# Kernel optimization log

Hardware: AMD Instinct MI355X
Metric: run time of the kernel (lower is better)

The kernel has to match this reference:

```python
import jax, jax.numpy as jnp
import numpy as np

U = 50  # lstm units

def lstm_seq(x, Wx, Wh, b):
    # x: [B,S,D] -> h: [B,S,U], Keras LSTMCell gate order i,f,g,o
    B = x.shape[0]
    xz = jnp.einsum('bsd,dk->bsk', x, Wx) + b  # [B,S,4U]
    def step(carry, zt):
        h, c = carry
        z = zt + h @ Wh
        i, f, g, o = jnp.split(z, 4, axis=-1)
        c = jax.nn.sigmoid(f) * c + jax.nn.sigmoid(i) * jnp.tanh(g)
        h = jax.nn.sigmoid(o) * jnp.tanh(c)
        return (h, c), h
    init = (jnp.zeros((B, U), x.dtype), jnp.zeros((B, U), x.dtype))
    _, hs = jax.lax.scan(step, init, jnp.swapaxes(xz, 0, 1))
    return jnp.swapaxes(hs, 0, 1)

def bilstm(x, fWx, fWh, fb, bWx, bWh, bb):
    # Keras RNN(go_backwards=True) does NOT re-reverse outputs; concat as-is.
    fw = lstm_seq(x, fWx, fWh, fb)
    bw = lstm_seq(x[:, ::-1, :], bWx, bWh, bb)
    return jnp.concatenate([fw, bw], axis=-1)

def local_inference(x1e, m1, x2e, m2):
    # Literal translation: inputs are batch-first [B,S,D]; the TF code transposes
    # to [S,B,D] and batch-matmuls over the leading (seq) axis, so attention is
    # over the batch index at each timestep. A[s,i,j] = x1e[i,s]. x2e[j,s]
    A = jnp.einsum('isd,jsd->sij', x1e, x2e)
    m1t = m1.T  # [S,B]
    m2t = m2.T
    w2 = jnp.exp(A - jnp.max(A, axis=2, keepdims=True)) * m2t[:, None, :]
    alpha = w2 / (jnp.sum(w2, axis=-1, keepdims=True) + 1e-8)
    x1_dual = jnp.einsum('sij,jsd->isd', alpha, x2e)  # [B,S,D]
    A1 = A - jnp.max(A, axis=1, keepdims=True)
    w1 = jnp.exp(jnp.swapaxes(A1, 1, 2)) * m1t[:, None, :]
    beta = w1 / (jnp.sum(w1, axis=-1, keepdims=True) + 1e-8)
    x2_dual = jnp.einsum('sji,isd->jsd', beta, x1e)  # [B,S,D]
    return x1_dual, x2_dual

def esim_forward(x1, x2, emb, b1f_Wx, b1f_Wh, b1f_b, b1b_Wx, b1b_Wh, b1b_b,
                 dense_W, dense_b, b2f_Wx, b2f_Wh, b2f_b, b2b_Wx, b2b_Wh, b2b_b,
                 dense1_W, dense1_b, out_W, out_b):
    m1 = (x1 != 0).astype(jnp.float32)
    m2 = (x2 != 0).astype(jnp.float32)
    e1 = emb[x1] * m1[..., None]
    e2 = emb[x2] * m2[..., None]
    enc1 = bilstm(e1, b1f_Wx, b1f_Wh, b1f_b, b1b_Wx, b1b_Wh, b1b_b) * m1[..., None]
    enc2 = bilstm(e2, b1f_Wx, b1f_Wh, b1f_b, b1b_Wx, b1b_Wh, b1b_b) * m2[..., None]
    d1, d2 = local_inference(enc1, m1, enc2, m2)
    match1 = jnp.concatenate([enc1, d1, enc1 * d1, enc1 - d1], axis=2)
    match2 = jnp.concatenate([enc2, d2, enc2 * d2, enc2 - d2], axis=2)
    map1 = jax.nn.relu(match1 @ dense_W + dense_b)
    map2 = jax.nn.relu(match2 @ dense_W + dense_b)
    cmp1 = bilstm(map1, b2f_Wx, b2f_Wh, b2f_b, b2b_Wx, b2b_Wh, b2b_b)
    cmp2 = bilstm(map2, b2f_Wx, b2f_Wh, b2f_b, b2b_Wx, b2b_Wh, b2b_b)
    c1m = cmp1 * m1[..., None]
    c2m = cmp2 * m2[..., None]
    p1_sum = jnp.sum(c1m, axis=1) / jnp.sum(m1, axis=1)[:, None]
    p1_max = jnp.max(c1m, axis=1)
    p2_sum = jnp.sum(c2m, axis=1) / jnp.sum(m2, axis=1)[:, None]
    p2_max = jnp.max(c2m, axis=1)
    logit = jnp.concatenate([p1_sum, p1_max, p2_sum, p2_max], axis=1)
    logit = jnp.tanh(logit @ dense1_W + dense1_b)
    logit = logit @ out_W + out_b
    return jax.nn.softmax(logit, axis=-1)

def setup_inputs() -> dict:
    key = jax.random.key(0)
    ks = jax.random.split(key, 24)
    B, S, V, E = 128, 512, 20000, 50
    def w(k, shape, s=0.05):
        return jax.random.normal(k, shape, dtype=jnp.float32) * s
    return {
        'x1': jax.random.randint(ks[0], (B, S), 0, V, dtype=jnp.int32),
        'x2': jax.random.randint(ks[1], (B, S), 0, V, dtype=jnp.int32),
        'emb': jax.random.uniform(ks[2], (V, E), jnp.float32, -0.05, 0.05),
        'b1f_Wx': w(ks[3], (E, 4 * U)), 'b1f_Wh': w(ks[4], (U, 4 * U)), 'b1f_b': w(ks[5], (4 * U,)),
        'b1b_Wx': w(ks[6], (E, 4 * U)), 'b1b_Wh': w(ks[7], (U, 4 * U)), 'b1b_b': w(ks[8], (4 * U,)),
        'dense_W': w(ks[9], (400, 100), 0.02), 'dense_b': jnp.zeros((100,), jnp.float32),
        'b2f_Wx': w(ks[10], (100, 4 * U)), 'b2f_Wh': w(ks[11], (U, 4 * U)), 'b2f_b': w(ks[12], (4 * U,)),
        'b2b_Wx': w(ks[13], (100, 4 * U)), 'b2b_Wh': w(ks[14], (U, 4 * U)), 'b2b_b': w(ks[15], (4 * U,)),
        'dense1_W': w(ks[16], (400, 100), 0.02), 'dense1_b': jnp.zeros((100,), jnp.float32),
        'out_W': w(ks[17], (100, 2), 0.02), 'out_b': jnp.zeros((2,), jnp.float32),
    }

def reference(x1, x2, emb, b1f_Wx, b1f_Wh, b1f_b, b1b_Wx, b1b_Wh, b1b_b,
              dense_W, dense_b, b2f_Wx, b2f_Wh, b2f_b, b2b_Wx, b2b_Wh, b2b_b,
              dense1_W, dense1_b, out_W, out_b):
    return esim_forward(x1, x2, emb, b1f_Wx, b1f_Wh, b1f_b, b1b_Wx, b1b_Wh, b1b_b,
                        dense_W, dense_b, b2f_Wx, b2f_Wh, b2f_b, b2b_Wx, b2b_Wh, b2b_b,
                        dense1_W, dense1_b, out_W, out_b)
```

## Files before the change

### kernel.cpp

```cpp
#include <hip/hip_runtime.h>

#define TOKN 65536
#define SQ 512
#define BB 128
#define DD 100
#define APAD 132

typedef unsigned short bf16t;
typedef __attribute__((ext_vector_type(8))) short bf16x8;
typedef __attribute__((ext_vector_type(4))) float floatx4;
typedef __attribute__((ext_vector_type(2))) _Float16 half2t;

__device__ __forceinline__ float bf2f(bf16t v) {
  unsigned u = ((unsigned)v) << 16;
  return __uint_as_float(u);
}
__device__ __forceinline__ bf16t f2bf(float x) {
  unsigned u = __float_as_uint(x);
  unsigned r = u + 0x7FFFu + ((u >> 16) & 1u);
  return (bf16t)(r >> 16);
}
__device__ __forceinline__ float2 ldpair(const float* p) { return *(const float2*)p; }
__device__ __forceinline__ float2 ldpair(const bf16t* p) {
  unsigned u = *(const unsigned*)p;
  float2 r;
  r.x = __uint_as_float(u << 16);
  r.y = __uint_as_float(u & 0xFFFF0000u);
  return r;
}
__device__ __forceinline__ half2t u2h2(unsigned u) {
  union { unsigned u; half2t h; } x; x.u = u; return x.h;
}

__device__ __forceinline__ float sigm(float x) { return 1.f / (1.f + __expf(-x)); }
__device__ __forceinline__ float tanhx(float x) { return 1.f - 2.f / (1.f + __expf(2.f * x)); }

#if __has_builtin(__builtin_amdgcn_fdot2)
#define DOT2(hu, wu, acc) acc = __builtin_amdgcn_fdot2(u2h2(hu), u2h2(wu), acc, false);
#else
#define DOT2(hu, wu, acc) { half2t hh = u2h2(hu), ww = u2h2(wu); \
  acc = fmaf((float)hh[0], (float)ww[0], acc); \
  acc = fmaf((float)hh[1], (float)ww[1], acc); }
#endif

__global__ __launch_bounds__(256) void embed_kernel(
    const int* __restrict__ x1, const int* __restrict__ x2,
    const float* __restrict__ emb,
    bf16t* __restrict__ e1, bf16t* __restrict__ e2,
    float* __restrict__ m1, float* __restrict__ m2) {
  const int which = blockIdx.y;
  const int* __restrict__ x = which ? x2 : x1;
  bf16t* __restrict__ e = which ? e2 : e1;
  float* __restrict__ m = which ? m2 : m1;
  int idx = blockIdx.x * 256 + threadIdx.x;
  int t = idx >> 6, d = idx & 63;
  int tok = x[t];
  float mk = (tok != 0) ? 1.f : 0.f;
  float v = (d < 50) ? emb[tok * 50 + d] * mk : 0.f;
  e[idx] = f2bf(v);
  if (d == 0) m[t] = mk;
}

__global__ __launch_bounds__(256) void padzero_kernel(
    unsigned* __restrict__ p1, unsigned* __restrict__ p2) {
  int idx = blockIdx.x * 256 + threadIdx.x;
  if (idx >= TOKN * 14) return;
  int t = idx / 14, d = idx - t * 14;
  p1[(size_t)t * 64 + 50 + d] = 0u;
  p2[(size_t)t * 64 + 50 + d] = 0u;
}

__global__ __launch_bounds__(256) void wprep_kernel(
    const float* __restrict__ w1f, const float* __restrict__ w1b,
    const float* __restrict__ w2f, const float* __restrict__ w2b,
    const float* __restrict__ dW,
    const float* __restrict__ h1f, const float* __restrict__ h1b,
    const float* __restrict__ h2f, const float* __restrict__ h2b,
    bf16t* __restrict__ w1T, bf16t* __restrict__ w2T, bf16t* __restrict__ wdT,
    unsigned* __restrict__ whP) {
  int idx = blockIdx.x * 256 + threadIdx.x;
  int sec = blockIdx.y;
  if (sec == 0) {
    if (idx >= 2 * 208 * 64) return;
    int d = idx / (208 * 64), r = idx % (208 * 64);
    int n = r >> 6, k = r & 63;
    const float* W = d ? w1b : w1f;
    float v = (n < 200 && k < 50) ? W[k * 200 + n] : 0.f;
    w1T[idx] = f2bf(v);
  } else if (sec == 1) {
    if (idx >= 2 * 208 * 128) return;
    int d = idx / (208 * 128), r = idx % (208 * 128);
    int n = r >> 7, k = r & 127;
    const float* W = d ? w2b : w2f;
    float v = (n < 200 && k < 100) ? W[k * 200 + n] : 0.f;
    w2T[idx] = f2bf(v);
  } else if (sec == 2) {
    if (idx >= 128 * 384) return;
    int n = idx / 384, kv = idx % 384;
    int reg = kv >> 7, kk = kv & 127;
    float v = 0.f;
    if (n < 100 && kk < 100) {
      if (reg == 0) v = dW[kk * 100 + n] + dW[(300 + kk) * 100 + n];
      else if (reg == 1) v = dW[(100 + kk) * 100 + n] - dW[(300 + kk) * 100 + n];
      else v = dW[(200 + kk) * 100 + n];
    }
    wdT[idx] = f2bf(v);
  } else {
    if (idx >= 4 * 25 * 200) return;
    int sd = idx / 5000, r = idx % 5000;
    int k2 = r / 200, colx = r % 200;
    const float* W = (sd == 0) ? h1f : (sd == 1) ? h1b : (sd == 2) ? h2f : h2b;
    float v0 = W[(2 * k2) * 200 + colx];
    float v1 = W[(2 * k2 + 1) * 200 + colx];
    union { _Float16 h[2]; unsigned u; } p;
    p.h[0] = (_Float16)v0;
    p.h[1] = (_Float16)v1;
    whP[idx] = p.u;
  }
}

template <int KP>
__global__ __launch_bounds__(256) void xz_mfma(
    const bf16t* __restrict__ A1, const bf16t* __restrict__ A2,
    const bf16t* __restrict__ WT,
    const float* __restrict__ bf_, const float* __restrict__ bb_,
    bf16t* __restrict__ out) {
  const int combo = blockIdx.y;
  const bf16t* __restrict__ A = (combo < 2) ? A1 : A2;
  const bf16t* __restrict__ W = WT + (size_t)(combo & 1) * 208 * KP;
  const float* __restrict__ bias = (combo & 1) ? bb_ : bf_;
  bf16t* __restrict__ O = out + (size_t)combo * TOKN * 200;
  const int tid = threadIdx.x;
  const int wave = tid >> 6, lane = tid & 63;
  const int m0 = blockIdx.x * 64 + wave * 16;
  const int l15 = lane & 15, quad = lane >> 4;
  floatx4 acc[13];
#pragma unroll
  for (int nt = 0; nt < 13; ++nt) acc[nt] = (floatx4){0.f, 0.f, 0.f, 0.f};
  const bf16t* __restrict__ arow = A + (size_t)(m0 + l15) * KP + quad * 8;
  const bf16t* __restrict__ wb = W + (size_t)l15 * KP + quad * 8;
#pragma unroll
  for (int ks = 0; ks < KP / 32; ++ks) {
    bf16x8 a = *(const bf16x8*)(arow + ks * 32);
#pragma unroll
    for (int nt = 0; nt < 13; ++nt) {
      bf16x8 b = *(const bf16x8*)(wb + (size_t)nt * 16 * KP + ks * 32);
      acc[nt] = __builtin_amdgcn_mfma_f32_16x16x32_bf16(a, b, acc[nt], 0, 0, 0);
    }
  }
  const int crow = m0 + quad * 4;
  const int bidx = crow >> 9;
  const int trow = crow & 511;
#pragma unroll
  for (int nt = 0; nt < 13; ++nt) {
    int n = nt * 16 + l15;
    if (n < 200) {
      float bn = bias[n];
      union { bf16t h[4]; uint2 u2; } pk;
#pragma unroll
      for (int r = 0; r < 4; ++r) pk.h[r] = f2bf(acc[nt][r] + bn);
      *(uint2*)&O[((size_t)bidx * 200 + n) * SQ + trow] = pk.u2;
    }
  }
}

__global__ __launch_bounds__(256) void dense_mfma(
    const bf16t* __restrict__ enc1, const bf16t* __restrict__ enc2,
    const bf16t* __restrict__ d1b, const bf16t* __restrict__ d2b,
    const bf16t* __restrict__ wdT, const float* __restrict__ bias,
    bf16t* __restrict__ map1, bf16t* __restrict__ map2) {
  const int inp = blockIdx.y;
  const bf16t* __restrict__ E = inp ? enc2 : enc1;
  const bf16t* __restrict__ Db = inp ? d2b : d1b;
  bf16t* __restrict__ O = inp ? map2 : map1;
  const int tid = threadIdx.x;
  const int wave = tid >> 6, lane = tid & 63;
  const int m0 = blockIdx.x * 64 + wave * 16;
  const int l15 = lane & 15, quad = lane >> 4;
  floatx4 acc[8];
#pragma unroll
  for (int nt = 0; nt < 8; ++nt) acc[nt] = (floatx4){0.f, 0.f, 0.f, 0.f};
  const bf16t* __restrict__ erow = E + (size_t)(m0 + l15) * 128 + quad * 8;
  const bf16t* __restrict__ drow = Db + (size_t)(m0 + l15) * 128 + quad * 8;
  const bf16t* __restrict__ wb = wdT + (size_t)l15 * 384 + quad * 8;
#pragma unroll
  for (int ks = 0; ks < 4; ++ks) {
    bf16x8 ae = *(const bf16x8*)(erow + ks * 32);
    bf16x8 ad = *(const bf16x8*)(drow + ks * 32);
    bf16x8 aed;
#pragma unroll
    for (int q = 0; q < 8; ++q) {
      float pe = bf2f((bf16t)ae[q]);
      float pd = bf2f((bf16t)ad[q]);
      aed[q] = (short)f2bf(pe * pd);
    }
#pragma unroll
    for (int nt = 0; nt < 8; ++nt) {
      const bf16t* wn = wb + (size_t)nt * 16 * 384 + ks * 32;
      bf16x8 b0 = *(const bf16x8*)(wn);
      acc[nt] = __builtin_amdgcn_mfma_f32_16x16x32_bf16(ae, b0, acc[nt], 0, 0, 0);
      bf16x8 b1 = *(const bf16x8*)(wn + 128);
      acc[nt] = __builtin_amdgcn_mfma_f32_16x16x32_bf16(ad, b1, acc[nt], 0, 0, 0);
      bf16x8 b2 = *(const bf16x8*)(wn + 256);
      acc[nt] = __builtin_amdgcn_mfma_f32_16x16x32_bf16(aed, b2, acc[nt], 0, 0, 0);
    }
  }
  const int crow = m0 + quad * 4;
#pragma unroll
  for (int nt = 0; nt < 8; ++nt) {
    int n = nt * 16 + l15;
    float bn = (n < 100) ? bias[n] : 0.f;
#pragma unroll
    for (int r = 0; r < 4; ++r) {
      float v = (n < 100) ? fmaxf(acc[nt][r] + bn, 0.f) : 0.f;
      O[(size_t)(crow + r) * 128 + n] = f2bf(v);
    }
  }
}

__global__ __launch_bounds__(64)
__attribute__((amdgpu_waves_per_eu(1, 2)))
void lstm_scan(
    const bf16t* __restrict__ xzT,
    const unsigned* __restrict__ whPL,
    bf16t* __restrict__ out1, bf16t* __restrict__ out2,
    const float* __restrict__ m1, const float* __restrict__ m2,
    int hasMask) {
  const int blk = blockIdx.x;
  const int scan = blk >> 7;
  const int b = blk & 127;
  const int inp = scan >> 1;
  const int dir = scan & 1;
  const int u = threadIdx.x;
  const bool act_l = (u < 50);
  const int uc = act_l ? u : 0;
  const bf16t* __restrict__ xbase = xzT + ((size_t)scan * 128 + b) * 200 * SQ;
  const bf16t* __restrict__ xi = xbase + (size_t)uc * SQ;
  const bf16t* __restrict__ xf = xbase + (size_t)(50 + uc) * SQ;
  const bf16t* __restrict__ xg = xbase + (size_t)(100 + uc) * SQ;
  const bf16t* __restrict__ xo = xbase + (size_t)(150 + uc) * SQ;
  bf16t* __restrict__ outp = (inp ? out2 : out1) + (size_t)b * SQ * 128 + dir * 50;
  const float* __restrict__ mk = (inp ? m2 : m1) + b * SQ;
  __shared__ __align__(16) unsigned hbuf[2][32];

  const unsigned* __restrict__ wsrc = whPL + dir * 5000;
  unsigned wgt[4][25];
#pragma unroll
  for (int gg = 0; gg < 4; ++gg)
#pragma unroll
    for (int k2 = 0; k2 < 25; ++k2)
      wgt[gg][k2] = wsrc[k2 * 200 + gg * 50 + uc];
#pragma unroll
  for (int gg = 0; gg < 4; ++gg)
#pragma unroll
    for (int k2 = 0; k2 < 25; ++k2)
      asm volatile("" : "+v"(wgt[gg][k2]));

  ((unsigned*)hbuf)[u] = 0;
  float c = 0.f;
  const float4* mk4 = (const float4*)mk;

  uint4 zc0, zc1, zc2, zc3, zn0, zn1, zn2, zn3;
  {
    int r0 = dir ? (SQ - 8) : 0;
    int r1 = dir ? (SQ - 16) : 8;
    zc0 = *(const uint4*)(xi + r0); zn0 = *(const uint4*)(xi + r1);
    zc1 = *(const uint4*)(xf + r0); zn1 = *(const uint4*)(xf + r1);
    zc2 = *(const uint4*)(xg + r0); zn2 = *(const uint4*)(xg + r1);
    zc3 = *(const uint4*)(xo + r0); zn3 = *(const uint4*)(xo + r1);
  }

  for (int g8 = 0; g8 < SQ / 8; ++g8) {
    float zst[4][8];
    {
      uint4 cur[4] = {zc0, zc1, zc2, zc3};
#pragma unroll
      for (int gg = 0; gg < 4; ++gg) {
        unsigned dw[4] = {cur[gg].x, cur[gg].y, cur[gg].z, cur[gg].w};
#pragma unroll
        for (int p = 0; p < 4; ++p) {
          float lo = __uint_as_float(dw[p] << 16);
          float hi = __uint_as_float(dw[p] & 0xFFFF0000u);
          if (dir) { zst[gg][7 - 2 * p] = lo; zst[gg][6 - 2 * p] = hi; }
          else     { zst[gg][2 * p] = lo;     zst[gg][2 * p + 1] = hi; }
        }
      }
    }
    uint4 zf0 = zn0, zf1 = zn1, zf2 = zn2, zf3 = zn3;
    {
      int gnext = (g8 + 2 < SQ / 8) ? (g8 + 2) : (SQ / 8 - 1);
      int rn = dir ? (SQ - 8 - 8 * gnext) : (8 * gnext);
      zn0 = *(const uint4*)(xi + rn);
      zn1 = *(const uint4*)(xf + rn);
      zn2 = *(const uint4*)(xg + rn);
      zn3 = *(const uint4*)(xo + rn);
    }
    float mva[8];
    if (hasMask) {
      float4 ma = mk4[2 * g8], mb = mk4[2 * g8 + 1];
      mva[0] = ma.x; mva[1] = ma.y; mva[2] = ma.z; mva[3] = ma.w;
      mva[4] = mb.x; mva[5] = mb.y; mva[6] = mb.z; mva[7] = mb.w;
    }
    bf16t hs8[8];
#pragma unroll
    for (int j = 0; j < 8; ++j) {
      const int par = j & 1;
      const uint4* hp = (const uint4*)&hbuf[par][0];
      uint4 q0 = hp[0], q1 = hp[1], q2 = hp[2], q3 = hp[3], q4 = hp[4], q5 = hp[5];
      unsigned qL = hbuf[par][24];
      unsigned hd[25] = {q0.x, q0.y, q0.z, q0.w, q1.x, q1.y, q1.z, q1.w,
                         q2.x, q2.y, q2.z, q2.w, q3.x, q3.y, q3.z, q3.w,
                         q4.x, q4.y, q4.z, q4.w, q5.x, q5.y, q5.z, q5.w, qL};
      float res[4];
#pragma unroll
      for (int gg = 0; gg < 4; ++gg) {
        float a0 = zst[gg][j], a1 = 0.f;
#pragma unroll
        for (int k2 = 0; k2 < 24; k2 += 2) {
          DOT2(hd[k2], wgt[gg][k2], a0)
          DOT2(hd[k2 + 1], wgt[gg][k2 + 1], a1)
        }
        DOT2(hd[24], wgt[gg][24], a0)
        res[gg] = a0 + a1;
      }
      float ai = sigm(res[0]);
      float af = sigm(res[1]);
      float ag = tanhx(res[2]);
      float ao = sigm(res[3]);
      c = af * c + ai * ag;
      float hn = ao * tanhx(c);
      if (act_l) {
        ((_Float16*)&hbuf[par ^ 1][0])[u] = (_Float16)hn;
        float mv = hasMask ? mva[j] : 1.f;
        hs8[j] = f2bf(hn * mv);
      }
    }
    if (act_l) {
      int t0 = 8 * g8;
#pragma unroll
      for (int j = 0; j < 8; ++j)
        outp[(size_t)(t0 + j) * 128 + u] = hs8[j];
    }
    zc0 = zf0; zc1 = zf1; zc2 = zf2; zc3 = zf3;
  }
}

__global__ __launch_bounds__(256) void attn_kernel(
    const bf16t* __restrict__ enc1, const bf16t* __restrict__ enc2,
    const float* __restrict__ m1, const float* __restrict__ m2,
    bf16t* __restrict__ d1b, bf16t* __restrict__ d2b) {
  const int s = blockIdx.x;
  const int tid = threadIdx.x;
  __shared__ __align__(16) float E1[BB][DD];
  __shared__ __align__(16) float E2[BB + 1][DD];
  __shared__ __align__(16) float Ah[64][APAD];
  __shared__ float mk1[BB], mk2[BB];
  __shared__ float rden[64];

  for (int idx = tid; idx < BB * 50; idx += 256) {
    int i = idx / 50, dp = idx - i * 50;
    float2 v1 = ldpair(enc1 + ((size_t)i * SQ + s) * 128 + 2 * dp);
    E1[i][2 * dp] = v1.x;
    E1[i][2 * dp + 1] = v1.y;
    float2 v2 = ldpair(enc2 + ((size_t)i * SQ + s) * 128 + 2 * dp);
    E2[i][2 * dp] = v2.x;
    E2[i][2 * dp + 1] = v2.y;
  }
  if (tid < BB) {
    mk1[tid] = m1[tid * SQ + s];
    mk2[tid] = m2[tid * SQ + s];
  }
  __syncthreads();

  const int ti = tid >> 4, tjj = tid & 15;
  const int xj = tid & 127;
  const int xd0 = (tid >> 7) * 50;
  float N[50];
#pragma unroll
  for (int q = 0; q < 50; ++q) N[q] = 0.f;
  float Dacc = 0.f, M = -1e30f;

  for (int half = 0; half < 2; ++half) {
    const int r0 = half * 64;
    float acc[4][8];
#pragma unroll
    for (int ii = 0; ii < 4; ++ii)
#pragma unroll
      for (int jj = 0; jj < 8; ++jj) acc[ii][jj] = 0.f;
    for (int k = 0; k < DD; k += 4) {
      float4 a4[4], b4[8];
#pragma unroll
      for (int ii = 0; ii < 4; ++ii)
        a4[ii] = *(const float4*)&E1[r0 + 4 * ti + ii][k];
#pragma unroll
      for (int jj = 0; jj < 8; ++jj)
        b4[jj] = *(const float4*)&E2[tjj + 16 * jj][k];
#pragma unroll
      for (int ii = 0; ii < 4; ++ii)
#pragma unroll
        for (int jj = 0; jj < 8; ++jj)
          acc[ii][jj] += a4[ii].x * b4[jj].x + a4[ii].y * b4[jj].y +
                         a4[ii].z * b4[jj].z + a4[ii].w * b4[jj].w;
    }
#pragma unroll
    for (int ii = 0; ii < 4; ++ii)
#pragma unroll
      for (int jj = 0; jj < 8; ++jj)
        Ah[4 * ti + ii][tjj + 16 * jj] = acc[ii][jj];
    __syncthreads();

    {
      float lm = M;
      for (int i = 0; i < 64; ++i) lm = fmaxf(lm, Ah[i][xj]);
      float scale = __expf(M - lm);
      Dacc *= scale;
#pragma unroll
      for (int q = 0; q < 50; ++q) N[q] *= scale;
      for (int i = 0; i < 64; ++i) {
        float p = __expf(Ah[i][xj] - lm) * mk1[r0 + i];
        Dacc += p;
        const float2* e1p = (const float2*)&E1[r0 + i][xd0];
#pragma unroll
        for (int q = 0; q < 25; ++q) {
          float2 ev = e1p[q];
          N[2 * q] += p * ev.x;
          N[2 * q + 1] += p * ev.y;
        }
      }
      M = lm;
    }
    __syncthreads();

    {
      int row = tid >> 2, seg = tid & 3;
      float mx = -1e30f;
      for (int q = 0; q < 32; ++q) mx = fmaxf(mx, Ah[row][seg + 4 * q]);
      mx = fmaxf(mx, __shfl_xor(mx, 1));
      mx = fmaxf(mx, __shfl_xor(mx, 2));
      float sm = 0.f;
      for (int q = 0; q < 32; ++q) {
        int jc = seg + 4 * q;
        float p = __expf(Ah[row][jc] - mx) * mk2[jc];
        Ah[row][jc] = p;
        sm += p;
      }
      sm += __shfl_xor(sm, 1);
      sm += __shfl_xor(sm, 2);
      if (seg == 0) rden[row] = sm + 1e-8f;
    }
    __syncthreads();

    {
      float o[4][8];
#pragma unroll
      for (int ii = 0; ii < 4; ++ii)
#pragma unroll
        for (int jj = 0; jj < 8; ++jj) o[ii][jj] = 0.f;
      for (int jb = 0; jb < BB; ++jb) {
        float pv[4], ev[8];
#pragma unroll
        for (int ii = 0; ii < 4; ++ii) pv[ii] = Ah[4 * ti + ii][jb];
#pragma unroll
        for (int jj = 0; jj < 8; ++jj) ev[jj] = E2[jb][tjj + 16 * jj];
#pragma unroll
        for (int ii = 0; ii < 4; ++ii)
#pragma unroll
          for (int jj = 0; jj < 8; ++jj) o[ii][jj] += pv[ii] * ev[jj];
      }
#pragma unroll
      for (int ii = 0; ii < 4; ++ii) {
        int i = r0 + 4 * ti + ii;
        float inv = 1.f / rden[4 * ti + ii];
#pragma unroll
        for (int jj = 0; jj < 8; ++jj) {
          int d = tjj + 16 * jj;
          float val = (d < DD) ? o[ii][jj] * inv : 0.f;
          d1b[((size_t)i * SQ + s) * 128 + d] = f2bf(val);
        }
      }
    }
    __syncthreads();
  }
  float invD = 1.f / (Dacc + 1e-8f);
#pragma unroll
  for (int q = 0; q < 50; ++q)
    d2b[((size_t)xj * SQ + s) * 128 + xd0 + q] = f2bf(N[q] * invD);
  if (xd0 == 50) {
#pragma unroll
    for (int q = 0; q < 28; ++q)
      d2b[((size_t)xj * SQ + s) * 128 + 100 + q] = 0;
  }
}

__global__ __launch_bounds__(128) void pool_kernel(
    const bf16t* __restrict__ cmp1, const bf16t* __restrict__ cmp2,
    const float* __restrict__ m1, const float* __restrict__ m2,
    float* __restrict__ pooled) {
  int b = blockIdx.x & 127, inp = blockIdx.x >> 7;
  const bf16t* C = (inp ? cmp2 : cmp1) + (size_t)b * SQ * 128;
  const float* M = (inp ? m2 : m1) + b * SQ;
  int f = threadIdx.x;
  float ms = 0.f;
  for (int s = f; s < SQ; s += 128) ms += M[s];
  __shared__ float red[128];
  red[f] = ms;
  __syncthreads();
  for (int o = 64; o > 0; o >>= 1) {
    if (f < o) red[f] += red[f + o];
    __syncthreads();
  }
  float msum = red[0];
  if (f < 100) {
    float sm = 0.f, mx = -1e30f;
    for (int s = 0; s < SQ; ++s) {
      float v = bf2f(C[(size_t)s * 128 + f]) * M[s];
      sm += v;
      mx = fmaxf(mx, v);
    }
    pooled[b * 400 + inp * 200 + f] = sm / msum;
    pooled[b * 400 + inp * 200 + 100 + f] = mx;
  }
}

__global__ __launch_bounds__(128) void final_kernel(
    const float* __restrict__ pooled, const float* __restrict__ W1,
    const float* __restrict__ b1, const float* __restrict__ W2,
    const float* __restrict__ b2, float* __restrict__ out) {
  int b = blockIdx.x;
  int j = threadIdx.x;
  __shared__ float pr[400];
  __shared__ float h[100];
  for (int idx = j; idx < 400; idx += 128) pr[idx] = pooled[b * 400 + idx];
  __syncthreads();
  if (j < 100) {
    float a = b1[j];
    for (int k = 0; k < 400; ++k) a += pr[k] * W1[k * 100 + j];
    h[j] = tanhx(a);
  }
  __syncthreads();
  if (j == 0) {
    float l0 = b2[0], l1 = b2[1];
    for (int k = 0; k < 100; ++k) {
      l0 += h[k] * W2[k * 2];
      l1 += h[k] * W2[k * 2 + 1];
    }
    float mx = fmaxf(l0, l1);
    float e0 = __expf(l0 - mx), e1 = __expf(l1 - mx);
    float inv = 1.f / (e0 + e1);
    out[b * 2] = e0 * inv;
    out[b * 2 + 1] = e1 * inv;
  }
}

extern "C" void kernel_launch(void* const* d_in, const int* in_sizes, int n_in,
                              void* d_out, int out_size, void* d_ws, size_t ws_size,
                              hipStream_t stream) {
  const int* x1 = (const int*)d_in[0];
  const int* x2 = (const int*)d_in[1];
  const float* emb = (const float*)d_in[2];
  const float* b1f_Wx = (const float*)d_in[3];
  const float* b1f_Wh = (const float*)d_in[4];
  const float* b1f_b = (const float*)d_in[5];
  const float* b1b_Wx = (const float*)d_in[6];
  const float* b1b_Wh = (const float*)d_in[7];
  const float* b1b_b = (const float*)d_in[8];
  const float* dense_W = (const float*)d_in[9];
  const float* dense_b = (const float*)d_in[10];
  const float* b2f_Wx = (const float*)d_in[11];
  const float* b2f_Wh = (const float*)d_in[12];
  const float* b2f_b = (const float*)d_in[13];
  const float* b2b_Wx = (const float*)d_in[14];
  const float* b2b_Wh = (const float*)d_in[15];
  const float* b2b_b = (const float*)d_in[16];
  const float* dense1_W = (const float*)d_in[17];
  const float* dense1_b = (const float*)d_in[18];
  const float* out_W = (const float*)d_in[19];
  const float* out_b = (const float*)d_in[20];
  float* out = (float*)d_out;

  char* base = (char*)d_ws;
  bf16t* xz = (bf16t*)base;
  bf16t* d1b = (bf16t*)base;
  bf16t* d2b = d1b + (size_t)TOKN * 128;
  char* r1 = base + (size_t)4 * TOKN * 200 * 2;
  bf16t* enc1 = (bf16t*)r1;
  bf16t* enc2 = enc1 + (size_t)TOKN * 128;
  bf16t* e1b = (bf16t*)r1;
  bf16t* e2b = e1b + (size_t)TOKN * 64;
  char* r2 = r1 + (size_t)2 * TOKN * 128 * 2;
  bf16t* map1 = (bf16t*)r2;
  bf16t* map2 = map1 + (size_t)TOKN * 128;
  char* r3 = r2 + (size_t)2 * TOKN * 128 * 2;
  float* m1 = (float*)r3;
  float* m2 = m1 + TOKN;
  float* pooled = m2 + TOKN;
  bf16t* w1T = (bf16t*)(r3 + ((size_t)2 * TOKN + 128 * 400) * 4);
  bf16t* w2T = w1T + 2 * 208 * 64;
  bf16t* wdT = w2T + 2 * 208 * 128;
  unsigned* whP = (unsigned*)(wdT + 128 * 384);
  bf16t* cmp1 = enc1;
  bf16t* cmp2 = enc2;
  (void)in_sizes; (void)n_in; (void)out_size; (void)ws_size;

  embed_kernel<<<dim3(TOKN * 64 / 256, 2), 256, 0, stream>>>(
      x1, x2, emb, e1b, e2b, m1, m2);
  wprep_kernel<<<dim3(208, 4), 256, 0, stream>>>(
      b1f_Wx, b1b_Wx, b2f_Wx, b2b_Wx, dense_W,
      b1f_Wh, b1b_Wh, b2f_Wh, b2b_Wh, w1T, w2T, wdT, whP);
  xz_mfma<64><<<dim3(TOKN / 64, 4), 256, 0, stream>>>(
      e1b, e2b, w1T, b1f_b, b1b_b, xz);
  padzero_kernel<<<(TOKN * 14 + 255) / 256, 256, 0, stream>>>(
      (unsigned*)enc1, (unsigned*)enc2);
  lstm_scan<<<512, 64, 0, stream>>>(xz, whP, enc1, enc2, m1, m2, 1);
  attn_kernel<<<SQ, 256, 0, stream>>>(enc1, enc2, m1, m2, d1b, d2b);
  dense_mfma<<<dim3(TOKN / 64, 2), 256, 0, stream>>>(
      enc1, enc2, d1b, d2b, wdT, dense_b, map1, map2);
  xz_mfma<128><<<dim3(TOKN / 64, 4), 256, 0, stream>>>(
      map1, map2, w2T, b2f_b, b2b_b, xz);
  lstm_scan<<<512, 64, 0, stream>>>(xz, whP + 2 * 5000, cmp1, cmp2, m1, m2, 0);
  pool_kernel<<<256, 128, 0, stream>>>(cmp1, cmp2, m1, m2, pooled);
  final_kernel<<<128, 128, 0, stream>>>(pooled, dense1_W, dense1_b, out_W, out_b, out);
}
```

Before: 1.055 ms.

## Split LSTM gates across two waves, each handling two batch rows

```diff
diff --git a/kernel.cpp b/kernel.cpp
--- a/kernel.cpp
+++ b/kernel.cpp
@@ -218,7 +218,7 @@
   }
 }
 
-__global__ __launch_bounds__(64)
+__global__ __launch_bounds__(128)
 __attribute__((amdgpu_waves_per_eu(1, 2)))
 void lstm_scan(
     const bf16t* __restrict__ xzT,
@@ -227,73 +227,64 @@
     const float* __restrict__ m1, const float* __restrict__ m2,
     int hasMask) {
   const int blk = blockIdx.x;
-  const int scan = blk >> 7;
-  const int b = blk & 127;
+  const int scan = blk >> 6;
+  const int pair = blk & 63;
   const int inp = scan >> 1;
   const int dir = scan & 1;
-  const int u = threadIdx.x;
+  const int tid = threadIdx.x;
+  const int w = tid >> 6;
+  const int u = tid & 63;
   const bool act_l = (u < 50);
   const int uc = act_l ? u : 0;
-  const bf16t* __restrict__ xbase = xzT + ((size_t)scan * 128 + b) * 200 * SQ;
-  const bf16t* __restrict__ xi = xbase + (size_t)uc * SQ;
-  const bf16t* __restrict__ xf = xbase + (size_t)(50 + uc) * SQ;
-  const bf16t* __restrict__ xg = xbase + (size_t)(100 + uc) * SQ;
-  const bf16t* __restrict__ xo = xbase + (size_t)(150 + uc) * SQ;
-  bf16t* __restrict__ outp = (inp ? out2 : out1) + (size_t)b * SQ * 128 + dir * 50;
-  const float* __restrict__ mk = (inp ? m2 : m1) + b * SQ;
-  __shared__ __align__(16) unsigned hbuf[2][32];
+  const int bA = pair, bB = pair + 64;
+  const int myB = w ? bB : bA;
+  const bf16t* __restrict__ xA0 =
+      xzT + (((size_t)scan * 128 + bA) * 200 + w * 100 + uc) * SQ;
+  const bf16t* __restrict__ xA1 = xA0 + (size_t)50 * SQ;
+  const bf16t* __restrict__ xB0 =
+      xzT + (((size_t)scan * 128 + bB) * 200 + w * 100 + uc) * SQ;
+  const bf16t* __restrict__ xB1 = xB0 + (size_t)50 * SQ;
+  bf16t* __restrict__ outp = (inp ? out2 : out1) + (size_t)myB * SQ * 128 + dir * 50;
+  const float* __restrict__ mk = (inp ? m2 : m1) + myB * SQ;
+  __shared__ __align__(16) unsigned hbuf[2][2][32];
+  __shared__ __align__(8) float2 actx[2][2][50];
 
   const unsigned* __restrict__ wsrc = whPL + dir * 5000;
-  unsigned wgt[4][25];
-#pragma unroll
-  for (int gg = 0; gg < 4; ++gg)
-#pragma unroll
-    for (int k2 = 0; k2 < 25; ++k2)
-      wgt[gg][k2] = wsrc[k2 * 200 + gg * 50 + uc];
-#pragma unroll
-  for (int gg = 0; gg < 4; ++gg)
-#pragma unroll
-    for (int k2 = 0; k2 < 25; ++k2)
-      asm volatile("" : "+v"(wgt[gg][k2]));
-
-  ((unsigned*)hbuf)[u] = 0;
+  unsigned wg0[25], wg1[25];
+#pragma unroll
+  for (int k2 = 0; k2 < 25; ++k2) {
+    wg0[k2] = wsrc[k2 * 200 + w * 100 + uc];
+    wg1[k2] = wsrc[k2 * 200 + w * 100 + 50 + uc];
+  }
+#pragma unroll
+  for (int k2 = 0; k2 < 25; ++k2) {
+    asm volatile("" : "+v"(wg0[k2]));
+    asm volatile("" : "+v"(wg1[k2]));
+  }
+
+  ((unsigned*)hbuf)[tid] = 0;
   float c = 0.f;
   const float4* mk4 = (const float4*)mk;
-
-  uint4 zc0, zc1, zc2, zc3, zn0, zn1, zn2, zn3;
-  {
-    int r0 = dir ? (SQ - 8) : 0;
-    int r1 = dir ? (SQ - 16) : 8;
-    zc0 = *(const uint4*)(xi + r0); zn0 = *(const uint4*)(xi + r1);
-    zc1 = *(const uint4*)(xf + r0); zn1 = *(const uint4*)(xf + r1);
-    zc2 = *(const uint4*)(xg + r0); zn2 = *(const uint4*)(xg + r1);
-    zc3 = *(const uint4*)(xo + r0); zn3 = *(const uint4*)(xo + r1);
-  }
+  __syncthreads();
 
   for (int g8 = 0; g8 < SQ / 8; ++g8) {
+    int r0 = dir ? (SQ - 8 - 8 * g8) : (8 * g8);
+    uint4 cur[4];
+    cur[0] = *(const uint4*)(xA0 + r0);
+    cur[1] = *(const uint4*)(xA1 + r0);
+    cur[2] = *(const uint4*)(xB0 + r0);
+    cur[3] = *(const uint4*)(xB1 + r0);
     float zst[4][8];
-    {
-      uint4 cur[4] = {zc0, zc1, zc2, zc3};
-#pragma unroll
-      for (int gg = 0; gg < 4; ++gg) {
-        unsigned dw[4] = {cur[gg].x, cur[gg].y, cur[gg].z, cur[gg].w};
-#pragma unroll
-        for (int p = 0; p < 4; ++p) {
-          float lo = __uint_as_float(dw[p] << 16);
-          float hi = __uint_as_float(dw[p] & 0xFFFF0000u);
-          if (dir) { zst[gg][7 - 2 * p] = lo; zst[gg][6 - 2 * p] = hi; }
-          else     { zst[gg][2 * p] = lo;     zst[gg][2 * p + 1] = hi; }
-        }
-      }
-    }
-    uint4 zf0 = zn0, zf1 = zn1, zf2 = zn2, zf3 = zn3;
-    {
-      int gnext = (g8 + 2 < SQ / 8) ? (g8 + 2) : (SQ / 8 - 1);
-      int rn = dir ? (SQ - 8 - 8 * gnext) : (8 * gnext);
-      zn0 = *(const uint4*)(xi + rn);
-      zn1 = *(const uint4*)(xf + rn);
-      zn2 = *(const uint4*)(xg + rn);
-      zn3 = *(const uint4*)(xo + rn);
+#pragma unroll
+    for (int gg = 0; gg < 4; ++gg) {
+      unsigned dw[4] = {cur[gg].x, cur[gg].y, cur[gg].z, cur[gg].w};
+#pragma unroll
+      for (int p = 0; p < 4; ++p) {
+        float lo = __uint_as_float(dw[p] << 16);
+        float hi = __uint_as_float(dw[p] & 0xFFFF0000u);
+        if (dir) { zst[gg][7 - 2 * p] = lo; zst[gg][6 - 2 * p] = hi; }
+        else     { zst[gg][2 * p] = lo;     zst[gg][2 * p + 1] = hi; }
+      }
     }
     float mva[8];
     if (hasMask) {
@@ -305,35 +296,63 @@
 #pragma unroll
     for (int j = 0; j < 8; ++j) {
       const int par = j & 1;
-      const uint4* hp = (const uint4*)&hbuf[par][0];
-      uint4 q0 = hp[0], q1 = hp[1], q2 = hp[2], q3 = hp[3], q4 = hp[4], q5 = hp[5];
-      unsigned qL = hbuf[par][24];
-      unsigned hd[25] = {q0.x, q0.y, q0.z, q0.w, q1.x, q1.y, q1.z, q1.w,
-                         q2.x, q2.y, q2.z, q2.w, q3.x, q3.y, q3.z, q3.w,
-                         q4.x, q4.y, q4.z, q4.w, q5.x, q5.y, q5.z, q5.w, qL};
-      float res[4];
-#pragma unroll
-      for (int gg = 0; gg < 4; ++gg) {
-        float a0 = zst[gg][j], a1 = 0.f;
-#pragma unroll
-        for (int k2 = 0; k2 < 24; k2 += 2) {
-          DOT2(hd[k2], wgt[gg][k2], a0)
-          DOT2(hd[k2 + 1], wgt[gg][k2 + 1], a1)
-        }
-        DOT2(hd[24], wgt[gg][24], a0)
-        res[gg] = a0 + a1;
-      }
-      float ai = sigm(res[0]);
-      float af = sigm(res[1]);
-      float ag = tanhx(res[2]);
-      float ao = sigm(res[3]);
-      c = af * c + ai * ag;
-      float hn = ao * tanhx(c);
+      const uint4* hA = (const uint4*)&hbuf[0][par][0];
+      uint4 a0 = hA[0], a1 = hA[1], a2 = hA[2], a3 = hA[3], a4 = hA[4], a5 = hA[5];
+      unsigned aL = hbuf[0][par][24];
+      const uint4* hB = (const uint4*)&hbuf[1][par][0];
+      uint4 b0 = hB[0], b1 = hB[1], b2 = hB[2], b3 = hB[3], b4 = hB[4], b5 = hB[5];
+      unsigned bL = hbuf[1][par][24];
+      unsigned hdA[25] = {a0.x, a0.y, a0.z, a0.w, a1.x, a1.y, a1.z, a1.w,
+                          a2.x, a2.y, a2.z, a2.w, a3.x, a3.y, a3.z, a3.w,
+                          a4.x, a4.y, a4.z, a4.w, a5.x, a5.y, a5.z, a5.w, aL};
+      unsigned hdB[25] = {b0.x, b0.y, b0.z, b0.w, b1.x, b1.y, b1.z, b1.w,
+                          b2.x, b2.y, b2.z, b2.w, b3.x, b3.y, b3.z, b3.w,
+                          b4.x, b4.y, b4.z, b4.w, b5.x, b5.y, b5.z, b5.w, bL};
+      float rA0a = zst[0][j], rA0b = 0.f;
+      float rA1a = zst[1][j], rA1b = 0.f;
+      float rB0a = zst[2][j], rB0b = 0.f;
+      float rB1a = zst[3][j], rB1b = 0.f;
+#pragma unroll
+      for (int k2 = 0; k2 < 24; k2 += 2) {
+        DOT2(hdA[k2], wg0[k2], rA0a)     DOT2(hdA[k2 + 1], wg0[k2 + 1], rA0b)
+        DOT2(hdA[k2], wg1[k2], rA1a)     DOT2(hdA[k2 + 1], wg1[k2 + 1], rA1b)
+        DOT2(hdB[k2], wg0[k2], rB0a)     DOT2(hdB[k2 + 1], wg0[k2 + 1], rB0b)
+        DOT2(hdB[k2], wg1[k2], rB1a)     DOT2(hdB[k2 + 1], wg1[k2 + 1], rB1b)
+      }
+      DOT2(hdA[24], wg0[24], rA0a)
+      DOT2(hdA[24], wg1[24], rA1a)
+      DOT2(hdB[24], wg0[24], rB0a)
+      DOT2(hdB[24], wg1[24], rB1a)
+      float rA0 = rA0a + rA0b, rA1 = rA1a + rA1b;
+      float rB0 = rB0a + rB0b, rB1 = rB1a + rB1b;
+      float a0A, a1A, a0B, a1B;
+      if (w == 0) {
+        a0A = sigm(rA0); a1A = sigm(rA1);
+        a0B = sigm(rB0); a1B = sigm(rB1);
+      } else {
+        a0A = tanhx(rA0); a1A = sigm(rA1);
+        a0B = tanhx(rB0); a1B = sigm(rB1);
+      }
       if (act_l) {
-        ((_Float16*)&hbuf[par ^ 1][0])[u] = (_Float16)hn;
+        actx[w][0][uc] = make_float2(a0A, a1A);
+        actx[w][1][uc] = make_float2(a0B, a1B);
+      }
+      __syncthreads();
+      if (act_l) {
+        float2 other = actx[w ^ 1][w][uc];
+        float myv0 = w ? a0B : a0A;
+        float myv1 = w ? a1B : a1A;
+        float iG = w ? other.x : myv0;
+        float fG = w ? other.y : myv1;
+        float gG = w ? myv0 : other.x;
+        float oG = w ? myv1 : other.y;
+        c = fG * c + iG * gG;
+        float hn = oG * tanhx(c);
+        ((_Float16*)&hbuf[w][par ^ 1][0])[u] = (_Float16)hn;
         float mv = hasMask ? mva[j] : 1.f;
         hs8[j] = f2bf(hn * mv);
       }
+      __syncthreads();
     }
     if (act_l) {
       int t0 = 8 * g8;
@@ -341,7 +360,6 @@
       for (int j = 0; j < 8; ++j)
         outp[(size_t)(t0 + j) * 128 + u] = hs8[j];
     }
-    zc0 = zf0; zc1 = zf1; zc2 = zf2; zc3 = zf3;
   }
 }
 
@@ -611,13 +629,13 @@
       e1b, e2b, w1T, b1f_b, b1b_b, xz);
   padzero_kernel<<<(TOKN * 14 + 255) / 256, 256, 0, stream>>>(
       (unsigned*)enc1, (unsigned*)enc2);
-  lstm_scan<<<512, 64, 0, stream>>>(xz, whP, enc1, enc2, m1, m2, 1);
+  lstm_scan<<<256, 128, 0, stream>>>(xz, whP, enc1, enc2, m1, m2, 1);
   attn_kernel<<<SQ, 256, 0, stream>>>(enc1, enc2, m1, m2, d1b, d2b);
   dense_mfma<<<dim3(TOKN / 64, 2), 256, 0, stream>>>(
       enc1, enc2, d1b, d2b, wdT, dense_b, map1, map2);
   xz_mfma<128><<<dim3(TOKN / 64, 4), 256, 0, stream>>>(
       map1, map2, w2T, b2f_b, b2b_b, xz);
-  lstm_scan<<<512, 64, 0, stream>>>(xz, whP + 2 * 5000, cmp1, cmp2, m1, m2, 0);
+  lstm_scan<<<256, 128, 0, stream>>>(xz, whP + 2 * 5000, cmp1, cmp2, m1, m2, 0);
   pool_kernel<<<256, 128, 0, stream>>>(cmp1, cmp2, m1, m2, pooled);
   final_kernel<<<128, 128, 0, stream>>>(pooled, dense1_W, dense1_b, out_W, out_b, out);
 }
```

Measured after the change: 1.267 ms. 20.1% more time.
